# Kernel optimization log

Hardware: AMD Instinct MI355X
Metric: run time of the kernel (lower is better)

The kernel has to match this reference:

```python
import jax, jax.numpy as jnp
import numpy as np

POOL_LIST = [1, 2, 3, 6]
NUM_ROIS = 32


def setup_inputs() -> dict:
    key = jax.random.key(0)
    k1, k2, k3, k4, k5 = jax.random.split(key, 5)
    feature_map = jax.random.normal(k1, (16, 96, 96, 512), dtype=jnp.float32)
    # rois = (x, y, w, h); keep crops fully in-bounds with bins >= 1 px at pool=6
    x = jax.random.randint(k2, (NUM_ROIS,), 0, 32)
    y = jax.random.randint(k3, (NUM_ROIS,), 0, 32)
    w = jax.random.randint(k4, (NUM_ROIS,), 8, 64)
    h = jax.random.randint(k5, (NUM_ROIS,), 8, 64)
    rois = jnp.stack([x, y, w, h], axis=1).astype(jnp.int32)
    return {"feature_map": feature_map, "rois": rois}


def reference(feature_map, rois):
    # Faithful port of RoiPooling.forward (note: the original swaps w/h when
    # computing col/row lengths; we reproduce that exactly).
    # ROI coords are index-like constants -> resolved on host for static slices.
    r = np.asarray(jax.device_get(rois))
    outputs = []
    for roi_idx in range(NUM_ROIS):
        x, y, w, h = (float(v) for v in r[roi_idx])
        row_length = [w / p for p in POOL_LIST]
        col_length = [h / p for p in POOL_LIST]
        for pool_num, num_pool_regions in enumerate(POOL_LIST):
            cl = col_length[pool_num]
            rl = row_length[pool_num]
            for ix in range(num_pool_regions):
                for jy in range(num_pool_regions):
                    x1 = int(round(x + ix * cl))
                    x2 = int(round(x + ix * cl + cl))
                    y1 = int(round(y + jy * rl))
                    y2 = int(round(y + jy * rl + rl))
                    crop = feature_map[:, y1:y2, x1:x2, :]  # (B, hy, wx, C)
                    outputs.append(jnp.max(crop, axis=(1, 2)))  # (B, C)
    out = jnp.stack(outputs)               # (num_rois*bins, B, C)
    return jnp.transpose(out, (1, 0, 2))   # (B, num_rois*bins, C)
```

## Files before the change

kernel.cpp:

```cpp
#include <hip/hip_runtime.h>
#include <math.h>

#define NUM_ROIS 32
#define REG_PER_ROI 50
#define FH 96
#define FW 96
#define FC 512
#define FC4 (FC / 4)
#define PIXB (FC * 4)
#define FB 16
#define NREG (NUM_ROIS * REG_PER_ROI)
#define NB6 36

__device__ __forceinline__ void atomic_max_f(float* a, float v) {
    if (v >= 0.0f) atomicMax((int*)a, __float_as_int(v));
    else           atomicMin((unsigned int*)a, __float_as_uint(v));
}

__device__ __forceinline__ float4 fmax4(float4 a, float4 b) {
    return make_float4(fmaxf(a.x,b.x), fmaxf(a.y,b.y),
                       fmaxf(a.z,b.z), fmaxf(a.w,b.w));
}

__global__ __launch_bounds__(128)
void roi_init_slots(float* __restrict__ out)
{
    const int roi = blockIdx.x, b = blockIdx.y;
    float4* out4 = (float4*)out;
    const size_t base = ((size_t)b*NREG + (size_t)roi*REG_PER_ROI)*FC4 + threadIdx.x;
    const float4 ninf = make_float4(-INFINITY,-INFINITY,-INFINITY,-INFINITY);
#pragma unroll
    for (int s = 1; s <= 13; ++s) out4[base + (size_t)s*FC4] = ninf;
}

__global__ __launch_bounds__(128)
void roi_pool_p6_cells(const float* __restrict__ fm,
                       const int* __restrict__ rois,
                       float* __restrict__ out)
{
    const int d   = blockIdx.x;
    const int wk  = (d & 7) * 144 + (d >> 3);
    const int roi = wk / NB6;
    const int l6  = wk % NB6;
    const int b   = blockIdx.y;

    const int ix = l6 / 6;
    const int jy = l6 % 6;

    const int rx = __builtin_amdgcn_readfirstlane(rois[roi * 4 + 0]);
    const int ry = __builtin_amdgcn_readfirstlane(rois[roi * 4 + 1]);
    const int rw = __builtin_amdgcn_readfirstlane(rois[roi * 4 + 2]);
    const int rh = __builtin_amdgcn_readfirstlane(rois[roi * 4 + 3]);

    const double cl6 = (double)rh / 6.0, rl6 = (double)rw / 6.0;
    const double cl3 = (double)rh / 3.0, rl3 = (double)rw / 3.0;
    const double xd = (double)rx, yd = (double)ry;

    const int X1 = (int)rint(xd + (double)ix * cl6);
    const int X2 = (int)rint(xd + (double)ix * cl6 + cl6);
    const int Y1 = (int)rint(yd + (double)jy * rl6);
    const int Y2 = (int)rint(yd + (double)jy * rl6 + rl6);
    const int XN = (ix < 5) ? (int)rint(xd + (double)(ix + 1) * cl6) : X2;
    const int YN = (jy < 5) ? (int)rint(yd + (double)(jy + 1) * rl6) : Y2;
    const int XE = X2 > XN ? X2 : XN;
    const int YE = Y2 > YN ? Y2 : YN;

    const int E2x  = (int)rint(xd + (double)rh * 0.5);
    const int E31x = (int)rint(xd + cl3);
    const int E32x = (int)rint(xd + 2.0 * cl3);
    const int E2y  = (int)rint(yd + (double)rw * 0.5);
    const int E31y = (int)rint(yd + rl3);
    const int E32y = (int)rint(yd + 2.0 * rl3);

    int xedg[6], yedg[6];
    int nxc, nyc;
    {
        int cut[4]; int nc = 0;
        auto addc = [&](int c, int lo, int hi) {
            if (c > lo && c < hi) {
                for (int t = 0; t < nc; ++t) if (cut[t] == c) return;
                cut[nc++] = c;
            }
        };
        nc = 0;
        addc(X2, X1, XE); addc(E2x, X1, XE); addc(E31x, X1, XE); addc(E32x, X1, XE);
        for (int a2 = 1; a2 < nc; ++a2) { int k = cut[a2], t = a2;
            while (t > 0 && cut[t-1] > k) { cut[t] = cut[t-1]; --t; } cut[t] = k; }
        xedg[0] = X1; for (int t = 0; t < nc; ++t) xedg[1+t] = cut[t];
        xedg[nc+1] = XE; nxc = nc + 1;

        nc = 0;
        addc(Y2, Y1, YE); addc(E2y, Y1, YE); addc(E31y, Y1, YE); addc(E32y, Y1, YE);
        for (int a2 = 1; a2 < nc; ++a2) { int k = cut[a2], t = a2;
            while (t > 0 && cut[t-1] > k) { cut[t] = cut[t-1]; --t; } cut[t] = k; }
        yedg[0] = Y1; for (int t = 0; t < nc; ++t) yedg[1+t] = cut[t];
        yedg[nc+1] = YE; nyc = nc + 1;
    }

    const int c4 = threadIdx.x;
    const int c4b = c4 * 16;
    const float* __restrict__ fmb = fm + (size_t)b * FH * FW * FC;
    const float4 ninf = make_float4(-INFINITY, -INFINITY, -INFINITY, -INFINITY);

#define ISSUE8(d0,d1,d2,d3,d4,d5,d6,d7, o0,o1,o2,o3,o4,o5,o6,o7, TAILW)       \
    asm volatile(                                                             \
        "global_load_dwordx4 %0, %8, %16\n\t"                                 \
        "global_load_dwordx4 %1, %9, %16\n\t"                                 \
        "global_load_dwordx4 %2, %10, %16\n\t"                                \
        "global_load_dwordx4 %3, %11, %16\n\t"                                \
        "global_load_dwordx4 %4, %12, %16\n\t"                                \
        "global_load_dwordx4 %5, %13, %16\n\t"                                \
        "global_load_dwordx4 %6, %14, %16\n\t"                                \
        "global_load_dwordx4 %7, %15, %16" TAILW                              \
        : "=&v"(d0), "=&v"(d1), "=&v"(d2), "=&v"(d3),                         \
          "=&v"(d4), "=&v"(d5), "=&v"(d6), "=&v"(d7)                          \
        : "v"(o0), "v"(o1), "v"(o2), "v"(o3),                                 \
          "v"(o4), "v"(o5), "v"(o6), "v"(o7),                                 \
          "s"(fmb))

#define CONS4(q0,q1,q2,q3)                                                    \
    do {                                                                      \
        a0.x=fmaxf(a0.x,q0.x); a0.y=fmaxf(a0.y,q0.y);                         \
        a0.z=fmaxf(a0.z,q0.z); a0.w=fmaxf(a0.w,q0.w);                         \
        a1.x=fmaxf(a1.x,q1.x); a1.y=fmaxf(a1.y,q1.y);                         \
        a1.z=fmaxf(a1.z,q1.z); a1.w=fmaxf(a1.w,q1.w);                         \
        a2.x=fmaxf(a2.x,q2.x); a2.y=fmaxf(a2.y,q2.y);                         \
        a2.z=fmaxf(a2.z,q2.z); a2.w=fmaxf(a2.w,q2.w);                         \
        a3.x=fmaxf(a3.x,q3.x); a3.y=fmaxf(a3.y,q3.y);                         \
        a3.z=fmaxf(a3.z,q3.z); a3.w=fmaxf(a3.w,q3.w);                         \
    } while (0)

    auto cellmax = [&](int ax0, int ax1, int ay0, int ay1) -> float4 {
        const int spanx = ax1 - ax0;
        const int n = spanx * (ay1 - ay0);
        const int rowjump = (FW - spanx) * PIXB;
        const int lastoff = ((ay1 - 1) * FW + (ax1 - 1)) * PIXB;
        int sx = ax0;
        int pixoff = (ay0 * FW + ax0) * PIXB;

        float4 a0 = ninf, a1 = ninf, a2 = ninf, a3 = ninf;
        float4 v0, v1, v2, v3, v4, v5, v6, v7;
        float4 w0, w1, w2, w3, w4, w5, w6, w7;

        for (int i = 0; i < n; i += 16) {
            int so[16];
#pragma unroll
            for (int t = 0; t < 16; ++t) {
                so[t] = (i + t < n) ? pixoff : lastoff;
                ++sx; pixoff += PIXB;
                if (sx == ax1) { sx = ax0; pixoff += rowjump; }
            }
            int vo[16];
#pragma unroll
            for (int t = 0; t < 16; ++t) vo[t] = c4b + so[t];

            ISSUE8(v0,v1,v2,v3,v4,v5,v6,v7,
                   vo[0],vo[1],vo[2],vo[3],vo[4],vo[5],vo[6],vo[7], );
            ISSUE8(w0,w1,w2,w3,w4,w5,w6,w7,
                   vo[8],vo[9],vo[10],vo[11],vo[12],vo[13],vo[14],vo[15],
                   "\n\ts_waitcnt vmcnt(0)");
            __builtin_amdgcn_sched_barrier(0);

            CONS4(v0, v1, v2, v3);
            CONS4(v4, v5, v6, v7);
            CONS4(w0, w1, w2, w3);
            CONS4(w4, w5, w6, w7);
        }
        float4 m;
        m.x = fmaxf(fmaxf(a0.x, a1.x), fmaxf(a2.x, a3.x));
        m.y = fmaxf(fmaxf(a0.y, a1.y), fmaxf(a2.y, a3.y));
        m.z = fmaxf(fmaxf(a0.z, a1.z), fmaxf(a2.z, a3.z));
        m.w = fmaxf(fmaxf(a0.w, a1.w), fmaxf(a2.w, a3.w));
        return m;
    };

    const size_t robase = (size_t)b * NREG + (size_t)roi * REG_PER_ROI;
    float4 accp6 = ninf;

    for (int cxi = 0; cxi < nxc; ++cxi) {
        const int ax0 = xedg[cxi], ax1 = xedg[cxi + 1];
        const bool inx = (ax1 <= X2);
        const int sx2 = (ax0 >= E2x) ? 2 : 0;
        const int ix3 = (ax0 >= E31x ? 1 : 0) + (ax0 >= E32x ? 1 : 0);
        for (int cyi = 0; cyi < nyc; ++cyi) {
            const int ay0 = yedg[cyi], ay1 = yedg[cyi + 1];
            const float4 mc = cellmax(ax0, ax1, ay0, ay1);

            if (inx && ay1 <= Y2) accp6 = fmax4(accp6, mc);

            const int s2 = 1 + sx2 + (ay0 >= E2y ? 1 : 0);
            const int s3 = 5 + ix3 * 3 + (ay0 >= E31y ? 1 : 0) + (ay0 >= E32y ? 1 : 0);
            float* p2 = out + ((robase + s2) * FC4 + c4) * 4;
            float* p3 = out + ((robase + s3) * FC4 + c4) * 4;
            atomic_max_f(p2 + 0, mc.x); atomic_max_f(p2 + 1, mc.y);
            atomic_max_f(p2 + 2, mc.z); atomic_max_f(p2 + 3, mc.w);
            atomic_max_f(p3 + 0, mc.x); atomic_max_f(p3 + 1, mc.y);
            atomic_max_f(p3 + 2, mc.z); atomic_max_f(p3 + 3, mc.w);
        }
    }
#undef ISSUE8
#undef CONS4

    float4* out4 = (float4*)out;
    out4[(robase + (14 + l6)) * FC4 + c4] = accp6;
}

__global__ __launch_bounds__(128)
void roi_pool_level0(float* __restrict__ out)
{
    const int roi = blockIdx.x;
    const int b   = blockIdx.y;
    const int c4  = threadIdx.x;

    float4* out4 = (float4*)out;
    const size_t base = ((size_t)b * NREG + (size_t)roi * REG_PER_ROI) * FC4 + c4;

    float4 a = out4[base + 1 * FC4];
    float4 c = out4[base + 2 * FC4];
    float4 d = out4[base + 3 * FC4];
    float4 e = out4[base + 4 * FC4];

    float4 m;
    m.x = fmaxf(fmaxf(a.x, c.x), fmaxf(d.x, e.x));
    m.y = fmaxf(fmaxf(a.y, c.y), fmaxf(d.y, e.y));
    m.z = fmaxf(fmaxf(a.z, c.z), fmaxf(d.z, e.z));
    m.w = fmaxf(fmaxf(a.w, c.w), fmaxf(d.w, e.w));

    out4[base] = m;
}

extern "C" void kernel_launch(void* const* d_in, const int* in_sizes, int n_in,
                              void* d_out, int out_size, void* d_ws, size_t ws_size,
                              hipStream_t stream) {
    const float* fm   = (const float*)d_in[0];
    const int*   rois = (const int*)d_in[1];
    float*       out  = (float*)d_out;

    dim3 grid0(NUM_ROIS, FB);
    roi_init_slots<<<grid0, dim3(128), 0, stream>>>(out);

    dim3 grid1(NUM_ROIS * NB6, FB);
    roi_pool_p6_cells<<<grid1, dim3(128), 0, stream>>>(fm, rois, out);

    dim3 grid2(NUM_ROIS, FB);
    roi_pool_level0<<<grid2, dim3(128), 0, stream>>>(out);
}
```

Baseline: 586.8 us.

## Assign one block per pool-3 bin covering four pool-6 bins, drop p3 atomics

```diff
diff --git a/kernel.cpp b/kernel.cpp
--- a/kernel.cpp
+++ b/kernel.cpp
@@ -10,7 +10,7 @@
 #define PIXB (FC * 4)
 #define FB 16
 #define NREG (NUM_ROIS * REG_PER_ROI)
-#define NB6 36
+#define NB3 9
 
 __device__ __forceinline__ void atomic_max_f(float* a, float v) {
     if (v >= 0.0f) atomicMax((int*)a, __float_as_int(v));
@@ -30,71 +30,93 @@
     const size_t base = ((size_t)b*NREG + (size_t)roi*REG_PER_ROI)*FC4 + threadIdx.x;
     const float4 ninf = make_float4(-INFINITY,-INFINITY,-INFINITY,-INFINITY);
 #pragma unroll
-    for (int s = 1; s <= 13; ++s) out4[base + (size_t)s*FC4] = ninf;
+    for (int s = 1; s <= 4; ++s) out4[base + (size_t)s*FC4] = ninf;
+}
+
+__device__ __forceinline__ int build_edges(int WS, int WE,
+                                           const int* cand, int ncand,
+                                           int* edg)
+{
+    int cut[7]; int nc = 0;
+    for (int t = 0; t < ncand; ++t) {
+        const int c = cand[t];
+        if (c > WS && c < WE) {
+            bool dup = false;
+            for (int u = 0; u < nc; ++u) if (cut[u] == c) dup = true;
+            if (!dup) cut[nc++] = c;
+        }
+    }
+    for (int a = 1; a < nc; ++a) { int k = cut[a], t = a;
+        while (t > 0 && cut[t-1] > k) { cut[t] = cut[t-1]; --t; } cut[t] = k; }
+    edg[0] = WS;
+    for (int t = 0; t < nc; ++t) edg[1 + t] = cut[t];
+    edg[nc + 1] = WE;
+    return nc + 1;
 }
 
 __global__ __launch_bounds__(128)
-void roi_pool_p6_cells(const float* __restrict__ fm,
+void roi_pool_p3_cells(const float* __restrict__ fm,
                        const int* __restrict__ rois,
                        float* __restrict__ out)
 {
     const int d   = blockIdx.x;
-    const int wk  = (d & 7) * 144 + (d >> 3);
-    const int roi = wk / NB6;
-    const int l6  = wk % NB6;
+    const int wk  = (d & 7) * 36 + (d >> 3);
+    const int roi = wk / NB3;
+    const int l3  = wk % NB3;
     const int b   = blockIdx.y;
 
-    const int ix = l6 / 6;
-    const int jy = l6 % 6;
+    const int i3 = l3 / 3;
+    const int j3 = l3 % 3;
+    const int kx0 = 2 * i3, ky0 = 2 * j3;
 
     const int rx = __builtin_amdgcn_readfirstlane(rois[roi * 4 + 0]);
     const int ry = __builtin_amdgcn_readfirstlane(rois[roi * 4 + 1]);
     const int rw = __builtin_amdgcn_readfirstlane(rois[roi * 4 + 2]);
     const int rh = __builtin_amdgcn_readfirstlane(rois[roi * 4 + 3]);
 
+    const double cl3 = (double)rh / 3.0, rl3 = (double)rw / 3.0;
     const double cl6 = (double)rh / 6.0, rl6 = (double)rw / 6.0;
-    const double cl3 = (double)rh / 3.0, rl3 = (double)rw / 3.0;
     const double xd = (double)rx, yd = (double)ry;
 
-    const int X1 = (int)rint(xd + (double)ix * cl6);
-    const int X2 = (int)rint(xd + (double)ix * cl6 + cl6);
-    const int Y1 = (int)rint(yd + (double)jy * rl6);
-    const int Y2 = (int)rint(yd + (double)jy * rl6 + rl6);
-    const int XN = (ix < 5) ? (int)rint(xd + (double)(ix + 1) * cl6) : X2;
-    const int YN = (jy < 5) ? (int)rint(yd + (double)(jy + 1) * rl6) : Y2;
-    const int XE = X2 > XN ? X2 : XN;
-    const int YE = Y2 > YN ? Y2 : YN;
-
+    const int A1x  = (int)rint(xd + (double)i3 * cl3);
+    const int A2x  = (int)rint(xd + (double)i3 * cl3 + cl3);
+    const int B1x0 = (int)rint(xd + (double)kx0 * cl6);
+    const int B2x0 = (int)rint(xd + (double)kx0 * cl6 + cl6);
+    const int B1x1 = (int)rint(xd + (double)(kx0 + 1) * cl6);
+    const int B2x1 = (int)rint(xd + (double)(kx0 + 1) * cl6 + cl6);
     const int E2x  = (int)rint(xd + (double)rh * 0.5);
-    const int E31x = (int)rint(xd + cl3);
-    const int E32x = (int)rint(xd + 2.0 * cl3);
+    int WSx = min(A1x, B1x0);
+    int WEx = max(A2x, B2x1);
+    if (i3 < 2) {
+        const int A1n = (int)rint(xd + (double)(i3 + 1) * cl3);
+        const int B1n = (int)rint(xd + (double)(kx0 + 2) * cl6);
+        const int Sn = min(A1n, B1n);
+        WEx = max(WEx, Sn);
+    }
+
+    const int A1y  = (int)rint(yd + (double)j3 * rl3);
+    const int A2y  = (int)rint(yd + (double)j3 * rl3 + rl3);
+    const int B1y0 = (int)rint(yd + (double)ky0 * rl6);
+    const int B2y0 = (int)rint(yd + (double)ky0 * rl6 + rl6);
+    const int B1y1 = (int)rint(yd + (double)(ky0 + 1) * rl6);
+    const int B2y1 = (int)rint(yd + (double)(ky0 + 1) * rl6 + rl6);
     const int E2y  = (int)rint(yd + (double)rw * 0.5);
-    const int E31y = (int)rint(yd + rl3);
-    const int E32y = (int)rint(yd + 2.0 * rl3);
-
-    int xedg[6], yedg[6];
+    int WSy = min(A1y, B1y0);
+    int WEy = max(A2y, B2y1);
+    if (j3 < 2) {
+        const int A1n = (int)rint(yd + (double)(j3 + 1) * rl3);
+        const int B1n = (int)rint(yd + (double)(ky0 + 2) * rl6);
+        const int Sn = min(A1n, B1n);
+        WEy = max(WEy, Sn);
+    }
+
+    int xedg[9], yedg[9];
     int nxc, nyc;
     {
-        int cut[4]; int nc = 0;
-        auto addc = [&](int c, int lo, int hi) {
-            if (c > lo && c < hi) {
-                for (int t = 0; t < nc; ++t) if (cut[t] == c) return;
-                cut[nc++] = c;
-            }
-        };
-        nc = 0;
-        addc(X2, X1, XE); addc(E2x, X1, XE); addc(E31x, X1, XE); addc(E32x, X1, XE);
-        for (int a2 = 1; a2 < nc; ++a2) { int k = cut[a2], t = a2;
-            while (t > 0 && cut[t-1] > k) { cut[t] = cut[t-1]; --t; } cut[t] = k; }
-        xedg[0] = X1; for (int t = 0; t < nc; ++t) xedg[1+t] = cut[t];
-        xedg[nc+1] = XE; nxc = nc + 1;
-
-        nc = 0;
-        addc(Y2, Y1, YE); addc(E2y, Y1, YE); addc(E31y, Y1, YE); addc(E32y, Y1, YE);
-        for (int a2 = 1; a2 < nc; ++a2) { int k = cut[a2], t = a2;
-            while (t > 0 && cut[t-1] > k) { cut[t] = cut[t-1]; --t; } cut[t] = k; }
-        yedg[0] = Y1; for (int t = 0; t < nc; ++t) yedg[1+t] = cut[t];
-        yedg[nc+1] = YE; nyc = nc + 1;
+        const int cx[7] = {A1x, A2x, B1x0, B2x0, B1x1, B2x1, E2x};
+        nxc = build_edges(WSx, WEx, cx, 7, xedg);
+        const int cy[7] = {A1y, A2y, B1y0, B2y0, B1y1, B2y1, E2y};
+        nyc = build_edges(WSy, WEy, cy, 7, yedg);
     }
 
     const int c4 = threadIdx.x;
@@ -174,35 +196,60 @@
         return m;
     };
 
-    const size_t robase = (size_t)b * NREG + (size_t)roi * REG_PER_ROI;
-    float4 accp6 = ninf;
+    float4 a6_00 = ninf, a6_01 = ninf, a6_10 = ninf, a6_11 = ninf;
+    float4 p3a   = ninf;
+    float4 p2_00 = ninf, p2_01 = ninf, p2_10 = ninf, p2_11 = ninf;
+    bool t00 = false, t01 = false, t10 = false, t11 = false;
 
     for (int cxi = 0; cxi < nxc; ++cxi) {
         const int ax0 = xedg[cxi], ax1 = xedg[cxi + 1];
-        const bool inx = (ax1 <= X2);
-        const int sx2 = (ax0 >= E2x) ? 2 : 0;
-        const int ix3 = (ax0 >= E31x ? 1 : 0) + (ax0 >= E32x ? 1 : 0);
+        const bool x60 = (ax0 >= B1x0) && (ax0 < B2x0);
+        const bool x61 = (ax0 >= B1x1) && (ax0 < B2x1);
+        const bool x3  = (ax0 >= A1x)  && (ax0 < A2x);
+        const bool px2 = (ax0 >= E2x);
         for (int cyi = 0; cyi < nyc; ++cyi) {
             const int ay0 = yedg[cyi], ay1 = yedg[cyi + 1];
+            const bool y60 = (ay0 >= B1y0) && (ay0 < B2y0);
+            const bool y61 = (ay0 >= B1y1) && (ay0 < B2y1);
+            const bool y3  = (ay0 >= A1y)  && (ay0 < A2y);
+            const bool py2 = (ay0 >= E2y);
+
             const float4 mc = cellmax(ax0, ax1, ay0, ay1);
 
-            if (inx && ay1 <= Y2) accp6 = fmax4(accp6, mc);
-
-            const int s2 = 1 + sx2 + (ay0 >= E2y ? 1 : 0);
-            const int s3 = 5 + ix3 * 3 + (ay0 >= E31y ? 1 : 0) + (ay0 >= E32y ? 1 : 0);
-            float* p2 = out + ((robase + s2) * FC4 + c4) * 4;
-            float* p3 = out + ((robase + s3) * FC4 + c4) * 4;
-            atomic_max_f(p2 + 0, mc.x); atomic_max_f(p2 + 1, mc.y);
-            atomic_max_f(p2 + 2, mc.z); atomic_max_f(p2 + 3, mc.w);
-            atomic_max_f(p3 + 0, mc.x); atomic_max_f(p3 + 1, mc.y);
-            atomic_max_f(p3 + 2, mc.z); atomic_max_f(p3 + 3, mc.w);
+            if (x3 && y3)   p3a   = fmax4(p3a,   mc);
+            if (x60 && y60) a6_00 = fmax4(a6_00, mc);
+            if (x60 && y61) a6_01 = fmax4(a6_01, mc);
+            if (x61 && y60) a6_10 = fmax4(a6_10, mc);
+            if (x61 && y61) a6_11 = fmax4(a6_11, mc);
+            if (!px2 && !py2) { p2_00 = fmax4(p2_00, mc); t00 = true; }
+            if (!px2 &&  py2) { p2_01 = fmax4(p2_01, mc); t01 = true; }
+            if ( px2 && !py2) { p2_10 = fmax4(p2_10, mc); t10 = true; }
+            if ( px2 &&  py2) { p2_11 = fmax4(p2_11, mc); t11 = true; }
         }
     }
 #undef ISSUE8
 #undef CONS4
 
+    const size_t robase = (size_t)b * NREG + (size_t)roi * REG_PER_ROI;
     float4* out4 = (float4*)out;
-    out4[(robase + (14 + l6)) * FC4 + c4] = accp6;
+
+    out4[(robase + 14 + (kx0 + 0) * 6 + (ky0 + 0)) * FC4 + c4] = a6_00;
+    out4[(robase + 14 + (kx0 + 0) * 6 + (ky0 + 1)) * FC4 + c4] = a6_01;
+    out4[(robase + 14 + (kx0 + 1) * 6 + (ky0 + 0)) * FC4 + c4] = a6_10;
+    out4[(robase + 14 + (kx0 + 1) * 6 + (ky0 + 1)) * FC4 + c4] = a6_11;
+    out4[(robase + 5 + i3 * 3 + j3) * FC4 + c4] = p3a;
+
+#define AT2(PX, PY, ACC, T)                                                   \
+    if (T) {                                                                  \
+        float* p = out + ((robase + 1 + (PX) * 2 + (PY)) * FC4 + c4) * 4;     \
+        atomic_max_f(p + 0, ACC.x); atomic_max_f(p + 1, ACC.y);               \
+        atomic_max_f(p + 2, ACC.z); atomic_max_f(p + 3, ACC.w);               \
+    }
+    AT2(0, 0, p2_00, t00)
+    AT2(0, 1, p2_01, t01)
+    AT2(1, 0, p2_10, t10)
+    AT2(1, 1, p2_11, t11)
+#undef AT2
 }
 
 __global__ __launch_bounds__(128)
@@ -239,8 +286,8 @@
     dim3 grid0(NUM_ROIS, FB);
     roi_init_slots<<<grid0, dim3(128), 0, stream>>>(out);
 
-    dim3 grid1(NUM_ROIS * NB6, FB);
-    roi_pool_p6_cells<<<grid1, dim3(128), 0, stream>>>(fm, rois, out);
+    dim3 grid1(NUM_ROIS * NB3, FB);
+    roi_pool_p3_cells<<<grid1, dim3(128), 0, stream>>>(fm, rois, out);
 
     dim3 grid2(NUM_ROIS, FB);
     roi_pool_level0<<<grid2, dim3(128), 0, stream>>>(out);
```

Measured after the change: 528.6 us. 1.11x faster.
